# Kernel optimization log

Measured on AMD Instinct MI355X. Metric: run time of the kernel, lower is better.

The kernel has to match this reference:

```python
import jax, jax.numpy as jnp
import numpy as np

N = 50000      # nodes
E = 800000     # edges
G = 2000       # graphs
F_IN = 34
HID = 256
H = 8
D = 32         # HID // H
L = 5


def _layer_norm(x, g, b, eps=1e-5):
    m = x.mean(-1, keepdims=True)
    v = ((x - m) ** 2).mean(-1, keepdims=True)
    return (x - m) / jnp.sqrt(v + eps) * g + b


def _gelu(x):
    return jax.nn.gelu(x, approximate=False)  # torch exact GELU


def _segment_softmax(scores, seg, n):
    # scores: [E', H], seg: [E'] target node ids
    m = jax.ops.segment_max(scores, seg, num_segments=n)
    m = jnp.where(jnp.isfinite(m), m, 0.0)
    ex = jnp.exp(scores - m[seg])
    den = jax.ops.segment_sum(ex, seg, num_segments=n)
    return ex / (den[seg] + 1e-16)


def setup_inputs() -> dict:
    key = jax.random.key(0)
    ks = iter(jax.random.split(key, 64))

    def p(shape, fan):
        return (jax.random.normal(next(ks), shape, jnp.float32) / np.sqrt(fan)).astype(jnp.float32)

    inp = {}
    inp['x'] = jax.random.normal(next(ks), (N, F_IN), jnp.float32)
    inp['edge_index'] = jax.random.randint(next(ks), (2, E), 0, N, jnp.int32)
    inp['batch'] = jnp.sort(jax.random.randint(next(ks), (N,), 0, G, jnp.int32))

    # input embed
    inp['in_W'] = p((F_IN, HID), F_IN); inp['in_b'] = jnp.zeros((HID,), jnp.float32)
    inp['in_ln_g'] = jnp.ones((HID,), jnp.float32); inp['in_ln_b'] = jnp.zeros((HID,), jnp.float32)
    # 5 GATv2 layers (stacked on leading dim)
    inp['gat_Wl'] = p((L, HID, HID), HID); inp['gat_bl'] = jnp.zeros((L, HID), jnp.float32)
    inp['gat_Wr'] = p((L, HID, HID), HID); inp['gat_br'] = jnp.zeros((L, HID), jnp.float32)
    inp['gat_att'] = p((L, H, D), D)
    inp['gat_bias'] = jnp.zeros((L, HID), jnp.float32)
    inp['gat_ln_g'] = jnp.ones((L, HID), jnp.float32); inp['gat_ln_b'] = jnp.zeros((L, HID), jnp.float32)
    # TransformerConv
    inp['tr_Wq'] = p((HID, HID), HID); inp['tr_bq'] = jnp.zeros((HID,), jnp.float32)
    inp['tr_Wk'] = p((HID, HID), HID); inp['tr_bk'] = jnp.zeros((HID,), jnp.float32)
    inp['tr_Wv'] = p((HID, HID), HID); inp['tr_bv'] = jnp.zeros((HID,), jnp.float32)
    inp['tr_Wskip'] = p((HID, HID), HID); inp['tr_bskip'] = jnp.zeros((HID,), jnp.float32)
    inp['tr_ln_g'] = jnp.ones((HID,), jnp.float32); inp['tr_ln_b'] = jnp.zeros((HID,), jnp.float32)
    # output proj
    inp['out_W'] = p((2 * HID, 2 * HID), 2 * HID); inp['out_b'] = jnp.zeros((2 * HID,), jnp.float32)
    inp['out_ln_g'] = jnp.ones((2 * HID,), jnp.float32); inp['out_ln_b'] = jnp.zeros((2 * HID,), jnp.float32)
    return inp


def reference(x, edge_index, batch,
              in_W, in_b, in_ln_g, in_ln_b,
              gat_Wl, gat_bl, gat_Wr, gat_br, gat_att, gat_bias, gat_ln_g, gat_ln_b,
              tr_Wq, tr_bq, tr_Wk, tr_bk, tr_Wv, tr_bv, tr_Wskip, tr_bskip, tr_ln_g, tr_ln_b,
              out_W, out_b, out_ln_g, out_ln_b):
    # input embedding (dropout inactive in eval)
    h = _gelu(_layer_norm(x @ in_W + in_b, in_ln_g, in_ln_b))

    src, dst = edge_index[0], edge_index[1]  # PyG: row=source j, col=target i
    loops = jnp.arange(N, dtype=src.dtype)
    s2 = jnp.concatenate([src, loops])  # GATv2 adds self loops
    d2 = jnp.concatenate([dst, loops])

    for l in range(L):  # small fixed loop over layers
        xl = (h @ gat_Wl[l] + gat_bl[l]).reshape(N, H, D)  # source transform / message
        xr = (h @ gat_Wr[l] + gat_br[l]).reshape(N, H, D)  # target transform
        e = jax.nn.leaky_relu(xl[s2] + xr[d2], 0.2)        # [E', H, D]
        score = jnp.einsum('ehd,hd->eh', e, gat_att[l])
        alpha = _segment_softmax(score, d2, N)             # softmax over incoming edges
        out = jax.ops.segment_sum(xl[s2] * alpha[..., None], d2, num_segments=N)
        out = out.reshape(N, HID) + gat_bias[l]
        h = h + _gelu(_layer_norm(out, gat_ln_g[l], gat_ln_b[l]))

    # TransformerConv (no self loops, root_weight skip connection)
    q = (h @ tr_Wq + tr_bq).reshape(N, H, D)
    k = (h @ tr_Wk + tr_bk).reshape(N, H, D)
    v = (h @ tr_Wv + tr_bv).reshape(N, H, D)
    score = (q[dst] * k[src]).sum(-1) / jnp.sqrt(jnp.float32(D))  # [E, H]
    alpha = _segment_softmax(score, dst, N)
    out = jax.ops.segment_sum(v[src] * alpha[..., None], dst, num_segments=N).reshape(N, HID)
    out = out + h @ tr_Wskip + tr_bskip
    h = h + _layer_norm(out, tr_ln_g, tr_ln_b)

    # global mean + max pool
    cnt = jax.ops.segment_sum(jnp.ones((N,), h.dtype), batch, num_segments=G)
    h_mean = jax.ops.segment_sum(h, batch, num_segments=G) / jnp.maximum(cnt, 1.0)[:, None]
    h_max = jax.ops.segment_max(h, batch, num_segments=G)
    h_max = jnp.where(jnp.isfinite(h_max), h_max, 0.0)
    ge = jnp.concatenate([h_mean, h_max], axis=-1)  # [G, 512]
    return _gelu(_layer_norm(ge @ out_W + out_b, out_ln_g, out_ln_b))
```

## Files before the change

### kernel.cpp

```cpp
#include <hip/hip_runtime.h>
#include <math.h>

#define N_NODES 50000
#define N_EDGES 800000
#define N_GRAPH 2000
#define F_INPUT 34
#define HID 256
#define NLAYER 5

typedef __attribute__((ext_vector_type(8))) short short8;
typedef __attribute__((ext_vector_type(4))) float float4v;

__device__ __forceinline__ float gelu_f(float x) {
  return 0.5f * x * (1.0f + erff(x * 0.70710678118654752440f));
}
__device__ __forceinline__ unsigned short bfr(float f) {
  unsigned u = __float_as_uint(f);
  return (unsigned short)((u + 0x7fffu + ((u >> 16) & 1u)) >> 16);
}
__device__ __forceinline__ float b2f(unsigned short s) {
  return __uint_as_float(((unsigned)s) << 16);
}
__device__ __forceinline__ float b2f_lo(unsigned u) {
  return __uint_as_float(u << 16);
}
__device__ __forceinline__ float b2f_hi(unsigned u) {
  return __uint_as_float(u & 0xffff0000u);
}
__device__ __forceinline__ float4 ld4bf(const unsigned short* p) {
  ushort4 u = *(const ushort4*)p;
  float4 f;
  f.x = b2f(u.x); f.y = b2f(u.y); f.z = b2f(u.z); f.w = b2f(u.w);
  return f;
}
__device__ __forceinline__ void acp16(const unsigned short* g, unsigned short* l) {
  __builtin_amdgcn_global_load_lds(
      (const __attribute__((address_space(1))) void*)g,
      (__attribute__((address_space(3))) void*)l, 16, 0, 0);
}

__global__ __launch_bounds__(256) void gemm_bias(
    const float* __restrict__ A, const float* __restrict__ B,
    const float* __restrict__ bias, float* __restrict__ C,
    int M, int Nn, int K) {
  __shared__ float As[16][64];
  __shared__ float Bs[16][64];
  int tid = threadIdx.x;
  int tx = tid & 15, ty = tid >> 4;
  int row0 = blockIdx.y * 64;
  int col0 = blockIdx.x * 64;
  float acc[4][4] = {};
  int a_r = tid >> 2;
  int a_c = (tid & 3) * 4;
  int b_r = tid >> 4;
  int b_c = (tid & 15) * 4;

  for (int k0 = 0; k0 < K; k0 += 16) {
    int ar = row0 + a_r;
#pragma unroll
    for (int i = 0; i < 4; ++i) {
      int kc = k0 + a_c + i;
      As[a_c + i][a_r] = (ar < M && kc < K) ? A[(long)ar * K + kc] : 0.f;
    }
    int bk = k0 + b_r;
    if (bk < K) {
      float4 bv = *(const float4*)&B[(long)bk * Nn + col0 + b_c];
      Bs[b_r][b_c + 0] = bv.x; Bs[b_r][b_c + 1] = bv.y;
      Bs[b_r][b_c + 2] = bv.z; Bs[b_r][b_c + 3] = bv.w;
    } else {
      Bs[b_r][b_c + 0] = 0.f; Bs[b_r][b_c + 1] = 0.f;
      Bs[b_r][b_c + 2] = 0.f; Bs[b_r][b_c + 3] = 0.f;
    }
    __syncthreads();
#pragma unroll
    for (int kk = 0; kk < 16; ++kk) {
      float4 a = *(const float4*)&As[kk][ty * 4];
      float4 b = *(const float4*)&Bs[kk][tx * 4];
      float av[4] = {a.x, a.y, a.z, a.w};
      float bv[4] = {b.x, b.y, b.z, b.w};
#pragma unroll
      for (int i = 0; i < 4; ++i)
#pragma unroll
        for (int j = 0; j < 4; ++j) acc[i][j] += av[i] * bv[j];
    }
    __syncthreads();
  }
  float4 bi = *(const float4*)&bias[col0 + tx * 4];
  float bia[4] = {bi.x, bi.y, bi.z, bi.w};
#pragma unroll
  for (int i = 0; i < 4; ++i) {
    int r = row0 + ty * 4 + i;
    if (r < M) {
      float4 o;
      o.x = acc[i][0] + bia[0]; o.y = acc[i][1] + bia[1];
      o.z = acc[i][2] + bia[2]; o.w = acc[i][3] + bia[3];
      *(float4*)&C[(long)r * Nn + col0 + tx * 4] = o;
    }
  }
}

__global__ __launch_bounds__(256) void gemm_mfma(
    const unsigned short* __restrict__ A, const unsigned short* __restrict__ Bt,
    const float* __restrict__ bias, void* __restrict__ Cv,
    int M, int Nn, int K, int flags) {
  __shared__ unsigned short smem[12288];
  unsigned short* As = smem;
  unsigned short* Bs = smem + 4096;
  int tid = threadIdx.x;
  int wave = tid >> 6, lane = tid & 63;

  int gx = gridDim.x;
  int flat = blockIdx.y * gx + blockIdx.x;
  int nwg = gx * gridDim.y;
  int xcd = flat & 7, idx = flat >> 3;
  int qb = nwg >> 3, r = nwg & 7;
  int g0 = xcd * qb + min(xcd, r);
  int wk = g0 + idx;
  int row0 = (wk / gx) * 128;
  int col0 = (wk % gx) * 128;

  int wm0 = (wave >> 1) * 64;
  int wn0 = (wave & 1) * 64;
  int q = lane >> 4;
  int ln = lane & 15;

  int srow = wave * 16 + (lane >> 2);
  int scol = (lane & 3) * 8;
  int ra0 = min(row0 + srow, M - 1);
  int ra1 = min(row0 + srow + 64, M - 1);
  const unsigned short* pa0 = A + (size_t)ra0 * K + scol;
  const unsigned short* pa1 = A + (size_t)ra1 * K + scol;
  const unsigned short* pb0 = Bt + (size_t)(col0 + srow) * K + scol;
  const unsigned short* pb1 = Bt + (size_t)(col0 + srow + 64) * K + scol;
  unsigned short* la0 = As + wave * 512;
  unsigned short* la1 = As + wave * 512 + 2048;
  unsigned short* lb0 = Bs + wave * 512;
  unsigned short* lb1 = Bs + wave * 512 + 2048;

  float4v acc[4][4];
#pragma unroll
  for (int i = 0; i < 4; ++i)
#pragma unroll
    for (int j = 0; j < 4; ++j) acc[i][j] = (float4v)0.f;

  for (int k0 = 0; k0 < K; k0 += 32) {
    acp16(pa0 + k0, la0);
    acp16(pa1 + k0, la1);
    acp16(pb0 + k0, lb0);
    acp16(pb1 + k0, lb1);
    __syncthreads();
    short8 af[4], bf[4];
#pragma unroll
    for (int i = 0; i < 4; ++i)
      af[i] = *(const short8*)&As[(wm0 + i * 16 + ln) * 32 + q * 8];
#pragma unroll
    for (int j = 0; j < 4; ++j)
      bf[j] = *(const short8*)&Bs[(wn0 + j * 16 + ln) * 32 + q * 8];
#pragma unroll
    for (int i = 0; i < 4; ++i)
#pragma unroll
      for (int j = 0; j < 4; ++j)
        acc[i][j] = __builtin_amdgcn_mfma_f32_16x16x32_bf16(af[i], bf[j], acc[i][j], 0, 0, 0);
    __syncthreads();
  }
  int rb = (lane >> 4) * 4;
  if (flags & 2) {
    unsigned short* Cb = (unsigned short*)Cv;
    unsigned short* eb = smem + wave * 2560;
#pragma unroll
    for (int p = 0; p < 2; ++p) {
#pragma unroll
      for (int jj = 0; jj < 2; ++jj) {
        int j = p * 2 + jj;
        float bv = bias[col0 + wn0 + j * 16 + ln];
#pragma unroll
        for (int i = 0; i < 4; ++i)
#pragma unroll
          for (int r2 = 0; r2 < 4; ++r2)
            eb[(i * 16 + rb + r2) * 40 + jj * 16 + ln] = bfr(acc[i][j][r2] + bv);
      }
      int grow = row0 + wm0 + lane;
      uint4 w0 = *(uint4*)&eb[lane * 40 + 0];
      uint4 w1 = *(uint4*)&eb[lane * 40 + 8];
      uint4 w2 = *(uint4*)&eb[lane * 40 + 16];
      uint4 w3 = *(uint4*)&eb[lane * 40 + 24];
      if (grow < M) {
        unsigned short* dst = Cb + (size_t)grow * Nn + col0 + wn0 + p * 32;
        *(uint4*)&dst[0] = w0;
        *(uint4*)&dst[8] = w1;
        *(uint4*)&dst[16] = w2;
        *(uint4*)&dst[24] = w3;
      }
    }
  } else {
    float* C = (float*)Cv;
#pragma unroll
    for (int j = 0; j < 4; ++j) {
      int col = col0 + wn0 + j * 16 + ln;
      float bv = bias[col];
#pragma unroll
      for (int i = 0; i < 4; ++i)
#pragma unroll
        for (int r2 = 0; r2 < 4; ++r2) {
          int row = row0 + wm0 + i * 16 + rb + r2;
          if (row < M) C[(size_t)row * Nn + col] = acc[i][j][r2] + bv;
        }
    }
  }
}

__global__ __launch_bounds__(256) void prep_w(
    const float* __restrict__ Wl, const float* __restrict__ Wr,
    const float* __restrict__ Wq, const float* __restrict__ Wk,
    const float* __restrict__ Wv, const float* __restrict__ Wsk,
    unsigned short* __restrict__ out) {
  __shared__ float t[32][33];
  int m = blockIdx.z;
  const float* W = (m < 10) ? (((m & 1) ? Wr : Wl) + (size_t)(m >> 1) * 65536)
                 : (m == 10) ? Wq : (m == 11) ? Wk : (m == 12) ? Wv : Wsk;
  int k0 = blockIdx.y * 32, n0 = blockIdx.x * 32;
  int r = threadIdx.x >> 5, c = threadIdx.x & 31;
  for (int rr = r; rr < 32; rr += 8)
    t[rr][c] = W[(size_t)(k0 + rr) * HID + n0 + c];
  __syncthreads();
  for (int rr = r; rr < 32; rr += 8) {
    int n = n0 + rr;
    size_t row;
    if (m == 11)      row = 11 * 256 + (size_t)((n >> 2) * 8 + (n & 3));
    else if (m == 12) row = 11 * 256 + (size_t)((n >> 2) * 8 + 4 + (n & 3));
    else              row = (size_t)m * 256 + n;
    out[row * HID + k0 + c] = bfr(t[c][rr]);
  }
}

__global__ __launch_bounds__(256) void prep_wout(const float* __restrict__ W,
                                                 unsigned short* __restrict__ o) {
  __shared__ float t[32][33];
  int k0 = blockIdx.y * 32, n0 = blockIdx.x * 32;
  int r = threadIdx.x >> 5, c = threadIdx.x & 31;
  for (int rr = r; rr < 32; rr += 8)
    t[rr][c] = W[(size_t)(k0 + rr) * 512 + n0 + c];
  __syncthreads();
  for (int rr = r; rr < 32; rr += 8)
    o[(size_t)(n0 + rr) * 512 + k0 + c] = bfr(t[c][rr]);
}

__global__ __launch_bounds__(256) void prep_bias(
    const float* __restrict__ bl, const float* __restrict__ br,
    const float* __restrict__ bq, const float* __restrict__ bk,
    const float* __restrict__ bv, const float* __restrict__ bsk,
    float* __restrict__ out) {
  int i = blockIdx.x * 256 + threadIdx.x;
  if (i < 2560) {
    int l = i >> 9, c = i & 511;
    out[i] = (c < 256) ? bl[l * 256 + c] : br[l * 256 + (c - 256)];
  } else if (i < 3584) {
    int j = i - 2560;
    float v;
    if (j < 256) {
      v = bq[j];
    } else if (j < 768) {
      int p = j - 256;
      int hi = p >> 3, lo = p & 7;
      v = (lo < 4) ? bk[hi * 4 + lo] : bv[hi * 4 + (lo - 4)];
    } else {
      v = bsk[j - 768];
    }
    out[i] = v;
  }
}

__global__ __launch_bounds__(256) void ln_act(
    const float* __restrict__ in, const float* __restrict__ gam,
    const float* __restrict__ bet, float* __restrict__ out,
    unsigned short* __restrict__ outb,
    int n_rows, int width, int do_gelu) {
  int wid = blockIdx.x * 4 + (threadIdx.x >> 6);
  int lane = threadIdx.x & 63;
  if (wid >= n_rows) return;
  int chunks = width >> 8;
  float4 v[2];
  float s = 0.f;
  for (int c = 0; c < chunks; ++c) {
    int off = c * 256 + lane * 4;
    float4 t = *(const float4*)&in[(size_t)wid * width + off];
    v[c] = t;
    s += t.x + t.y + t.z + t.w;
  }
  for (int o = 1; o < 64; o <<= 1) s += __shfl_xor(s, o);
  float mean = s / (float)width;
  float vs = 0.f;
  for (int c = 0; c < chunks; ++c) {
    float dx = v[c].x - mean, dy = v[c].y - mean, dz = v[c].z - mean, dw = v[c].w - mean;
    vs += dx * dx + dy * dy + dz * dz + dw * dw;
  }
  for (int o = 1; o < 64; o <<= 1) vs += __shfl_xor(vs, o);
  float inv = rsqrtf(vs / (float)width + 1e-5f);
  for (int c = 0; c < chunks; ++c) {
    int off = c * 256 + lane * 4;
    float4 g4 = *(const float4*)&gam[off];
    float4 b4 = *(const float4*)&bet[off];
    float y[4] = {(v[c].x - mean) * inv * g4.x + b4.x,
                  (v[c].y - mean) * inv * g4.y + b4.y,
                  (v[c].z - mean) * inv * g4.z + b4.z,
                  (v[c].w - mean) * inv * g4.w + b4.w};
    if (do_gelu) {
#pragma unroll
      for (int i = 0; i < 4; ++i) y[i] = gelu_f(y[i]);
    }
    size_t idx = (size_t)wid * width + off;
    float4 o4 = {y[0], y[1], y[2], y[3]};
    *(float4*)&out[idx] = o4;
    if (outb) {
      ushort4 ob = {bfr(y[0]), bfr(y[1]), bfr(y[2]), bfr(y[3])};
      *(ushort4*)&outb[idx] = ob;
    }
  }
}

__global__ __launch_bounds__(256) void edge_count(const int* __restrict__ ei,
                                                  int* __restrict__ counts) {
  int e = blockIdx.x * 256 + threadIdx.x;
  if (e < N_EDGES) atomicAdd(&counts[ei[N_EDGES + e]], 1);
}

__global__ __launch_bounds__(1024) void scan1(const int* __restrict__ counts,
                                              int* __restrict__ indptr,
                                              int* __restrict__ bsums, int n) {
  __shared__ int sm[1024];
  int tid = threadIdx.x;
  int i = blockIdx.x * 1024 + tid;
  int v = (i < n) ? counts[i] : 0;
  sm[tid] = v;
  __syncthreads();
  for (int off = 1; off < 1024; off <<= 1) {
    int t = (tid >= off) ? sm[tid - off] : 0;
    __syncthreads();
    sm[tid] += t;
    __syncthreads();
  }
  if (i < n) indptr[i] = sm[tid] - v;
  if (tid == 1023) bsums[blockIdx.x] = sm[1023];
}

__global__ void scan2(int* __restrict__ bsums, int nb) {
  if (threadIdx.x == 0 && blockIdx.x == 0) {
    int acc = 0;
    for (int i = 0; i < nb; ++i) { int t = bsums[i]; bsums[i] = acc; acc += t; }
  }
}

__global__ __launch_bounds__(256) void scan3(const int* __restrict__ bsums,
                                             int* __restrict__ indptr,
                                             int* __restrict__ cursor, int n) {
  int i = blockIdx.x * 256 + threadIdx.x;
  if (i < n) {
    int v = indptr[i] + bsums[i >> 10];
    indptr[i] = v;
    cursor[i] = v;
  }
  if (i == 0) indptr[n] = N_EDGES;
}

__global__ __launch_bounds__(256) void edge_scatter(const int* __restrict__ ei,
                                                    int* __restrict__ cursor,
                                                    int* __restrict__ esrc) {
  int e = blockIdx.x * 256 + threadIdx.x;
  if (e < N_EDGES) {
    int d = ei[N_EDGES + e];
    int p = atomicAdd(&cursor[d], 1);
    esrc[p] = ei[e];
  }
}

#define GAT_EDGE(f)                                                        \
  {                                                                        \
    float ex = f.x + xri.x; ex = fmaxf(ex, 0.2f * ex);                     \
    float ey = f.y + xri.y; ey = fmaxf(ey, 0.2f * ey);                     \
    float ez = f.z + xri.z; ez = fmaxf(ez, 0.2f * ez);                     \
    float ew = f.w + xri.w; ew = fmaxf(ew, 0.2f * ew);                     \
    float p = ex * a4.x + ey * a4.y + ez * a4.z + ew * a4.w;               \
    p += __shfl_xor(p, 1); p += __shfl_xor(p, 2); p += __shfl_xor(p, 4);   \
    float wgt = __expf(fminf(p - m0, 60.f));                               \
    ax = fmaf(wgt, f.x, ax); ay = fmaf(wgt, f.y, ay);                      \
    az = fmaf(wgt, f.z, az); aw = fmaf(wgt, f.w, aw);                      \
    lsum += wgt;                                                           \
  }

__global__ __launch_bounds__(256) void gat_agg(
    const unsigned short* __restrict__ xlr, const float* __restrict__ att,
    const int* __restrict__ indptr, const int* __restrict__ esrc,
    const float* __restrict__ pre_bias, const float* __restrict__ gam,
    const float* __restrict__ bet, float* __restrict__ h,
    unsigned short* __restrict__ hb) {
  int wid = blockIdx.x * 4 + (threadIdx.x >> 6);
  int lane = threadIdx.x & 63;
  if (wid >= N_NODES) return;
  float4 xri = ld4bf(&xlr[(size_t)wid * 512 + 256 + lane * 4]);
  float4 a4 = *(const float4*)&att[lane * 4];
  int beg = indptr[wid], end = indptr[wid + 1];

  float m0, lsum, ax, ay, az, aw;
  {
    float4 f = ld4bf(&xlr[(size_t)wid * 512 + lane * 4]);
    float ex = f.x + xri.x; ex = fmaxf(ex, 0.2f * ex);
    float ey = f.y + xri.y; ey = fmaxf(ey, 0.2f * ey);
    float ez = f.z + xri.z; ez = fmaxf(ez, 0.2f * ez);
    float ew = f.w + xri.w; ew = fmaxf(ew, 0.2f * ew);
    float p = ex * a4.x + ey * a4.y + ez * a4.z + ew * a4.w;
    p += __shfl_xor(p, 1); p += __shfl_xor(p, 2); p += __shfl_xor(p, 4);
    m0 = p; lsum = 1.f;
    ax = f.x; ay = f.y; az = f.z; aw = f.w;
  }
  const unsigned short* xbase = xlr + lane * 4;
  int e = beg;
  for (; e + 3 < end; e += 4) {
    int j0 = esrc[e], j1 = esrc[e + 1], j2 = esrc[e + 2], j3 = esrc[e + 3];
    float4 f0 = ld4bf(xbase + (size_t)j0 * 512);
    float4 f1 = ld4bf(xbase + (size_t)j1 * 512);
    float4 f2 = ld4bf(xbase + (size_t)j2 * 512);
    float4 f3 = ld4bf(xbase + (size_t)j3 * 512);
    GAT_EDGE(f0); GAT_EDGE(f1); GAT_EDGE(f2); GAT_EDGE(f3);
  }
  for (; e < end; ++e) {
    int j = esrc[e];
    float4 f = ld4bf(xbase + (size_t)j * 512);
    GAT_EDGE(f);
  }
  float inv = 1.f / (lsum + 1e-16f);
  float4 pb = *(const float4*)&pre_bias[lane * 4];
  float y0 = ax * inv + pb.x, y1 = ay * inv + pb.y;
  float y2 = az * inv + pb.z, y3 = aw * inv + pb.w;
  float s = y0 + y1 + y2 + y3;
  for (int o = 1; o < 64; o <<= 1) s += __shfl_xor(s, o);
  float mean = s * (1.f / 256.f);
  float d0 = y0 - mean, d1 = y1 - mean, d2 = y2 - mean, d3 = y3 - mean;
  float vs = d0 * d0 + d1 * d1 + d2 * d2 + d3 * d3;
  for (int o = 1; o < 64; o <<= 1) vs += __shfl_xor(vs, o);
  float inv2 = rsqrtf(vs * (1.f / 256.f) + 1e-5f);
  float4 g4 = *(const float4*)&gam[lane * 4];
  float4 b4 = *(const float4*)&bet[lane * 4];
  y0 = gelu_f(d0 * inv2 * g4.x + b4.x);
  y1 = gelu_f(d1 * inv2 * g4.y + b4.y);
  y2 = gelu_f(d2 * inv2 * g4.z + b4.z);
  y3 = gelu_f(d3 * inv2 * g4.w + b4.w);
  size_t idx = (size_t)wid * HID + lane * 4;
  float4 r4 = *(const float4*)&h[idx];
  y0 += r4.x; y1 += r4.y; y2 += r4.z; y3 += r4.w;
  float4 o4 = {y0, y1, y2, y3};
  *(float4*)&h[idx] = o4;
  ushort4 ob = {bfr(y0), bfr(y1), bfr(y2), bfr(y3)};
  *(ushort4*)&hb[idx] = ob;
}

#define TR_EDGE(u_)                                                         \
  {                                                                         \
    float p = qi.x * b2f_lo(u_.x);                                          \
    p = fmaf(qi.y, b2f_hi(u_.x), p);                                        \
    p = fmaf(qi.z, b2f_lo(u_.y), p);                                        \
    p = fmaf(qi.w, b2f_hi(u_.y), p);                                        \
    p += __shfl_xor(p, 1); p += __shfl_xor(p, 2); p += __shfl_xor(p, 4);    \
    float wgt = __expf(fminf(p, 60.f));                                     \
    ax = fmaf(wgt, b2f_lo(u_.z), ax); ay = fmaf(wgt, b2f_hi(u_.z), ay);     \
    az = fmaf(wgt, b2f_lo(u_.w), az); aw = fmaf(wgt, b2f_hi(u_.w), aw);     \
    lsum += wgt;                                                            \
  }

__global__ __launch_bounds__(256) void tr_agg(
    const unsigned short* __restrict__ qkv, const int* __restrict__ indptr,
    const int* __restrict__ esrc,
    const float* __restrict__ gam, const float* __restrict__ bet,
    float* __restrict__ h) {
  int wid = blockIdx.x * 4 + (threadIdx.x >> 6);
  int lane = threadIdx.x & 63;
  if (wid >= N_NODES) return;
  const float scale = 0.17677669529663687f;
  float4 qi = ld4bf(&qkv[(size_t)wid * 1024 + lane * 4]);
  qi.x *= scale; qi.y *= scale; qi.z *= scale; qi.w *= scale;
  const unsigned short* kvbase = qkv + 256 + lane * 8;
  int beg = indptr[wid], end = indptr[wid + 1];
  float lsum = 0.f;
  float ax = 0.f, ay = 0.f, az = 0.f, aw = 0.f;
  int e = beg;
  for (; e + 3 < end; e += 4) {
    int j0 = esrc[e], j1 = esrc[e + 1], j2 = esrc[e + 2], j3 = esrc[e + 3];
    uint4 u0 = *(const uint4*)(kvbase + (size_t)j0 * 1024);
    uint4 u1 = *(const uint4*)(kvbase + (size_t)j1 * 1024);
    uint4 u2 = *(const uint4*)(kvbase + (size_t)j2 * 1024);
    uint4 u3 = *(const uint4*)(kvbase + (size_t)j3 * 1024);
    TR_EDGE(u0); TR_EDGE(u1); TR_EDGE(u2); TR_EDGE(u3);
  }
  for (; e < end; ++e) {
    uint4 u0 = *(const uint4*)(kvbase + (size_t)esrc[e] * 1024);
    TR_EDGE(u0);
  }
  float inv = 1.f / (lsum + 1e-16f);
  size_t idx = (size_t)wid * HID + lane * 4;
  float4 sk = ld4bf(&qkv[(size_t)wid * 1024 + 768 + lane * 4]);
  float y0 = ax * inv + sk.x, y1 = ay * inv + sk.y;
  float y2 = az * inv + sk.z, y3 = aw * inv + sk.w;
  float s = y0 + y1 + y2 + y3;
  for (int o = 1; o < 64; o <<= 1) s += __shfl_xor(s, o);
  float mean = s * (1.f / 256.f);
  float d0 = y0 - mean, d1 = y1 - mean, d2 = y2 - mean, d3 = y3 - mean;
  float vs = d0 * d0 + d1 * d1 + d2 * d2 + d3 * d3;
  for (int o = 1; o < 64; o <<= 1) vs += __shfl_xor(vs, o);
  float inv2 = rsqrtf(vs * (1.f / 256.f) + 1e-5f);
  float4 g4 = *(const float4*)&gam[lane * 4];
  float4 b4 = *(const float4*)&bet[lane * 4];
  float4 r4 = *(const float4*)&h[idx];
  float4 o4;
  o4.x = r4.x + d0 * inv2 * g4.x + b4.x;
  o4.y = r4.y + d1 * inv2 * g4.y + b4.y;
  o4.z = r4.z + d2 * inv2 * g4.z + b4.z;
  o4.w = r4.w + d3 * inv2 * g4.w + b4.w;
  *(float4*)&h[idx] = o4;
}

__global__ __launch_bounds__(256) void graph_bounds(const int* __restrict__ batch,
                                                    int* __restrict__ gptr) {
  int i = blockIdx.x * 256 + threadIdx.x;
  if (i >= N_NODES) return;
  int b0 = batch[i];
  if (i == 0)
    for (int g = 0; g <= b0; ++g) gptr[g] = 0;
  int b1 = (i + 1 < N_NODES) ? batch[i + 1] : N_GRAPH;
  for (int g = b0 + 1; g <= b1; ++g) gptr[g] = i + 1;
}

__global__ __launch_bounds__(256) void pool_seg(
    const float* __restrict__ h, const int* __restrict__ gptr,
    unsigned short* __restrict__ geb) {
  int g = blockIdx.x, c = threadIdx.x;
  int s = gptr[g], e = gptr[g + 1];
  float sum = 0.f, mx = -INFINITY;
  for (int r = s; r < e; ++r) {
    float vv = h[(size_t)r * HID + c];
    sum += vv;
    mx = fmaxf(mx, vv);
  }
  int cnt = e - s;
  geb[(size_t)g * 512 + c] = bfr(sum / (float)max(cnt, 1));
  geb[(size_t)g * 512 + 256 + c] = bfr(cnt ? mx : 0.f);
}

static inline void mfma_launch(const unsigned short* A, const unsigned short* Bt,
                               const float* bias, void* C, int M, int Nn, int K,
                               int flags, hipStream_t s) {
  dim3 grid(Nn / 128, (M + 127) / 128);
  gemm_mfma<<<grid, 256, 0, s>>>(A, Bt, bias, C, M, Nn, K, flags);
}

extern "C" void kernel_launch(void* const* d_in, const int* in_sizes, int n_in,
                              void* d_out, int out_size, void* d_ws, size_t ws_size,
                              hipStream_t stream) {
  const float* x       = (const float*)d_in[0];
  const int*   ei      = (const int*)d_in[1];
  const int*   batch   = (const int*)d_in[2];
  const float* in_W    = (const float*)d_in[3];
  const float* in_b    = (const float*)d_in[4];
  const float* in_ln_g = (const float*)d_in[5];
  const float* in_ln_b = (const float*)d_in[6];
  const float* gat_Wl  = (const float*)d_in[7];
  const float* gat_bl  = (const float*)d_in[8];
  const float* gat_Wr  = (const float*)d_in[9];
  const float* gat_br  = (const float*)d_in[10];
  const float* gat_att = (const float*)d_in[11];
  const float* gat_bias= (const float*)d_in[12];
  const float* gat_ln_g= (const float*)d_in[13];
  const float* gat_ln_b= (const float*)d_in[14];
  const float* tr_Wq   = (const float*)d_in[15];
  const float* tr_bq   = (const float*)d_in[16];
  const float* tr_Wk   = (const float*)d_in[17];
  const float* tr_bk   = (const float*)d_in[18];
  const float* tr_Wv   = (const float*)d_in[19];
  const float* tr_bv   = (const float*)d_in[20];
  const float* tr_Wsk  = (const float*)d_in[21];
  const float* tr_bsk  = (const float*)d_in[22];
  const float* tr_ln_g = (const float*)d_in[23];
  const float* tr_ln_b = (const float*)d_in[24];
  const float* out_W   = (const float*)d_in[25];
  const float* out_b   = (const float*)d_in[26];
  const float* out_ln_g= (const float*)d_in[27];
  const float* out_ln_b= (const float*)d_in[28];

  char* w = (char*)d_ws;
  auto take = [&](size_t bytes) -> char* {
    char* p = w;
    w += (bytes + 255) & ~(size_t)255;
    return p;
  };
  const size_t NB = (size_t)N_NODES * HID * sizeof(float);
  float* h    = (float*)take(NB);
  float* aggO = (float*)take(NB);
  unsigned short* hb  = (unsigned short*)take((size_t)N_NODES * HID * 2);
  unsigned short* xq  = (unsigned short*)take((size_t)N_NODES * 1024 * 2);
  unsigned short* wbuf= (unsigned short*)take((size_t)(14 * 65536 + 262144) * 2);
  float* bcat = (float*)take(3584 * sizeof(float));
  int* indptr = (int*)take((N_NODES + 1) * sizeof(int));
  int* cursor = (int*)take(N_NODES * sizeof(int));
  int* counts = (int*)take(N_NODES * sizeof(int));
  int* esrc   = (int*)take(N_EDGES * sizeof(int));
  int* bsums  = (int*)take(64 * sizeof(int));
  char* w2 = (char*)xq;
  auto take2 = [&](size_t bytes) -> char* {
    char* p = w2;
    w2 += (bytes + 255) & ~(size_t)255;
    return p;
  };
  int* gptr = (int*)take2((N_GRAPH + 1) * sizeof(int));
  unsigned short* geb = (unsigned short*)take2((size_t)N_GRAPH * 512 * 2);
  float* tbuf = (float*)take2((size_t)N_GRAPH * 512 * sizeof(float));

  const int EB = (N_EDGES + 255) / 256;
  const int WB = (N_NODES + 3) / 4;
  const int NSB = (N_NODES + 1023) / 1024;

  {
    dim3 g(8, 8, 14);
    prep_w<<<g, 256, 0, stream>>>(gat_Wl, gat_Wr, tr_Wq, tr_Wk, tr_Wv, tr_Wsk, wbuf);
    dim3 g2(16, 16);
    prep_wout<<<g2, 256, 0, stream>>>(out_W, wbuf + (size_t)14 * 65536);
    prep_bias<<<14, 256, 0, stream>>>(gat_bl, gat_br, tr_bq, tr_bk, tr_bv, tr_bsk, bcat);
  }

  hipMemsetAsync(counts, 0, N_NODES * sizeof(int), stream);
  edge_count<<<EB, 256, 0, stream>>>(ei, counts);
  scan1<<<NSB, 1024, 0, stream>>>(counts, indptr, bsums, N_NODES);
  scan2<<<1, 64, 0, stream>>>(bsums, NSB);
  scan3<<<(N_NODES + 255) / 256, 256, 0, stream>>>(bsums, indptr, cursor, N_NODES);
  edge_scatter<<<EB, 256, 0, stream>>>(ei, cursor, esrc);

  {
    dim3 grid(HID / 64, (N_NODES + 63) / 64);
    gemm_bias<<<grid, 256, 0, stream>>>(x, in_W, in_b, aggO, N_NODES, HID, F_INPUT);
  }
  ln_act<<<WB, 256, 0, stream>>>(aggO, in_ln_g, in_ln_b, h, hb, N_NODES, HID, 1);

  for (int l = 0; l < NLAYER; ++l) {
    mfma_launch(hb, wbuf + (size_t)(2 * l) * 65536, bcat + l * 512, xq,
                N_NODES, 512, HID, 2, stream);
    gat_agg<<<WB, 256, 0, stream>>>(xq, gat_att + l * HID, indptr, esrc,
                                    gat_bias + l * HID, gat_ln_g + l * HID,
                                    gat_ln_b + l * HID, h, hb);
  }

  mfma_launch(hb, wbuf + (size_t)10 * 65536, bcat + 2560, xq,
              N_NODES, 1024, HID, 2, stream);
  tr_agg<<<WB, 256, 0, stream>>>(xq, indptr, esrc, tr_ln_g, tr_ln_b, h);

  graph_bounds<<<(N_NODES + 255) / 256, 256, 0, stream>>>(batch, gptr);
  pool_seg<<<N_GRAPH, 256, 0, stream>>>(h, gptr, geb);

  mfma_launch(geb, wbuf + (size_t)14 * 65536, out_b, tbuf,
              N_GRAPH, 512, 512, 0, stream);
  ln_act<<<(N_GRAPH + 3) / 4, 256, 0, stream>>>(tbuf, out_ln_g, out_ln_b,
                                                (float*)d_out, nullptr,
                                                N_GRAPH, 512, 1);
}
```

Baseline: 1.138 ms.

## Fuse input embed with layernorm, deepen MFMA K tile, merge prep and scan kernels

Replaces the generic fp32 input GEMM plus separate layernorm/GELU pass with one fused kernel that computes the 34-wide projection, layernorm and GELU per 16-row tile, removing an intermediate N×256 buffer round trip. The MFMA GEMM now stages a 64-wide K slice per iteration, halving barrier count at the cost of more LDS. The three weight and bias prep kernels are merged into one launch, and the single-thread scan2 is folded into scan3, where each block sums its preceding block totals. These cut launch overhead and memory traffic but add redundant prefix work per block.

```diff
diff --git a/kernel.cpp b/kernel.cpp
--- a/kernel.cpp
+++ b/kernel.cpp
@@ -39,63 +39,66 @@
       (__attribute__((address_space(3))) void*)l, 16, 0, 0);
 }
 
-__global__ __launch_bounds__(256) void gemm_bias(
-    const float* __restrict__ A, const float* __restrict__ B,
-    const float* __restrict__ bias, float* __restrict__ C,
-    int M, int Nn, int K) {
-  __shared__ float As[16][64];
-  __shared__ float Bs[16][64];
+__global__ __launch_bounds__(256) void embed_fused(
+    const float* __restrict__ x, const float* __restrict__ W,
+    const float* __restrict__ bias, const float* __restrict__ gam,
+    const float* __restrict__ bet, float* __restrict__ h,
+    unsigned short* __restrict__ hb) {
+  __shared__ float xs[16][34];
+  __shared__ float ys[16][256];
   int tid = threadIdx.x;
-  int tx = tid & 15, ty = tid >> 4;
-  int row0 = blockIdx.y * 64;
-  int col0 = blockIdx.x * 64;
-  float acc[4][4] = {};
-  int a_r = tid >> 2;
-  int a_c = (tid & 3) * 4;
-  int b_r = tid >> 4;
-  int b_c = (tid & 15) * 4;
-
-  for (int k0 = 0; k0 < K; k0 += 16) {
-    int ar = row0 + a_r;
-#pragma unroll
-    for (int i = 0; i < 4; ++i) {
-      int kc = k0 + a_c + i;
-      As[a_c + i][a_r] = (ar < M && kc < K) ? A[(long)ar * K + kc] : 0.f;
-    }
-    int bk = k0 + b_r;
-    if (bk < K) {
-      float4 bv = *(const float4*)&B[(long)bk * Nn + col0 + b_c];
-      Bs[b_r][b_c + 0] = bv.x; Bs[b_r][b_c + 1] = bv.y;
-      Bs[b_r][b_c + 2] = bv.z; Bs[b_r][b_c + 3] = bv.w;
-    } else {
-      Bs[b_r][b_c + 0] = 0.f; Bs[b_r][b_c + 1] = 0.f;
-      Bs[b_r][b_c + 2] = 0.f; Bs[b_r][b_c + 3] = 0.f;
-    }
-    __syncthreads();
-#pragma unroll
-    for (int kk = 0; kk < 16; ++kk) {
-      float4 a = *(const float4*)&As[kk][ty * 4];
-      float4 b = *(const float4*)&Bs[kk][tx * 4];
-      float av[4] = {a.x, a.y, a.z, a.w};
-      float bv[4] = {b.x, b.y, b.z, b.w};
-#pragma unroll
-      for (int i = 0; i < 4; ++i)
-#pragma unroll
-        for (int j = 0; j < 4; ++j) acc[i][j] += av[i] * bv[j];
-    }
-    __syncthreads();
-  }
-  float4 bi = *(const float4*)&bias[col0 + tx * 4];
-  float bia[4] = {bi.x, bi.y, bi.z, bi.w};
-#pragma unroll
-  for (int i = 0; i < 4; ++i) {
-    int r = row0 + ty * 4 + i;
-    if (r < M) {
-      float4 o;
-      o.x = acc[i][0] + bia[0]; o.y = acc[i][1] + bia[1];
-      o.z = acc[i][2] + bia[2]; o.w = acc[i][3] + bia[3];
-      *(float4*)&C[(long)r * Nn + col0 + tx * 4] = o;
-    }
+  int r0 = blockIdx.x * 16;
+  float* xsf = &xs[0][0];
+  for (int i = tid; i < 544; i += 256) xsf[i] = x[(size_t)r0 * 34 + i];
+  __syncthreads();
+  {
+    int rr = tid >> 4;
+    int c0 = (tid & 15) * 16;
+    float acc[16];
+#pragma unroll
+    for (int j = 0; j < 16; j += 4) {
+      float4 b4 = *(const float4*)&bias[c0 + j];
+      acc[j] = b4.x; acc[j + 1] = b4.y; acc[j + 2] = b4.z; acc[j + 3] = b4.w;
+    }
+    for (int k = 0; k < 34; ++k) {
+      float xv = xs[rr][k];
+#pragma unroll
+      for (int j = 0; j < 16; j += 4) {
+        float4 w4 = *(const float4*)&W[(size_t)k * 256 + c0 + j];
+        acc[j]     = fmaf(xv, w4.x, acc[j]);
+        acc[j + 1] = fmaf(xv, w4.y, acc[j + 1]);
+        acc[j + 2] = fmaf(xv, w4.z, acc[j + 2]);
+        acc[j + 3] = fmaf(xv, w4.w, acc[j + 3]);
+      }
+    }
+#pragma unroll
+    for (int j = 0; j < 16; j += 4) {
+      float4 o = {acc[j], acc[j + 1], acc[j + 2], acc[j + 3]};
+      *(float4*)&ys[rr][c0 + j] = o;
+    }
+  }
+  __syncthreads();
+  int wv = tid >> 6, lane = tid & 63;
+  for (int rr = wv * 4; rr < wv * 4 + 4; ++rr) {
+    float4 v = *(const float4*)&ys[rr][lane * 4];
+    float s = v.x + v.y + v.z + v.w;
+    for (int o = 1; o < 64; o <<= 1) s += __shfl_xor(s, o);
+    float mean = s * (1.f / 256.f);
+    float d0 = v.x - mean, d1 = v.y - mean, d2 = v.z - mean, d3 = v.w - mean;
+    float vs = d0 * d0 + d1 * d1 + d2 * d2 + d3 * d3;
+    for (int o = 1; o < 64; o <<= 1) vs += __shfl_xor(vs, o);
+    float inv = rsqrtf(vs * (1.f / 256.f) + 1e-5f);
+    float4 g4 = *(const float4*)&gam[lane * 4];
+    float4 b4 = *(const float4*)&bet[lane * 4];
+    float y0 = gelu_f(d0 * inv * g4.x + b4.x);
+    float y1 = gelu_f(d1 * inv * g4.y + b4.y);
+    float y2 = gelu_f(d2 * inv * g4.z + b4.z);
+    float y3 = gelu_f(d3 * inv * g4.w + b4.w);
+    size_t idx = (size_t)(r0 + rr) * HID + lane * 4;
+    float4 o4 = {y0, y1, y2, y3};
+    *(float4*)&h[idx] = o4;
+    ushort4 ob = {bfr(y0), bfr(y1), bfr(y2), bfr(y3)};
+    *(ushort4*)&hb[idx] = ob;
   }
 }
 
@@ -103,9 +106,9 @@
     const unsigned short* __restrict__ A, const unsigned short* __restrict__ Bt,
     const float* __restrict__ bias, void* __restrict__ Cv,
     int M, int Nn, int K, int flags) {
-  __shared__ unsigned short smem[12288];
+  __shared__ unsigned short smem[16384];
   unsigned short* As = smem;
-  unsigned short* Bs = smem + 4096;
+  unsigned short* Bs = smem + 8192;
   int tid = threadIdx.x;
   int wave = tid >> 6, lane = tid & 63;
 
@@ -124,18 +127,20 @@
   int q = lane >> 4;
   int ln = lane & 15;
 
-  int srow = wave * 16 + (lane >> 2);
-  int scol = (lane & 3) * 8;
-  int ra0 = min(row0 + srow, M - 1);
-  int ra1 = min(row0 + srow + 64, M - 1);
-  const unsigned short* pa0 = A + (size_t)ra0 * K + scol;
-  const unsigned short* pa1 = A + (size_t)ra1 * K + scol;
-  const unsigned short* pb0 = Bt + (size_t)(col0 + srow) * K + scol;
-  const unsigned short* pb1 = Bt + (size_t)(col0 + srow + 64) * K + scol;
-  unsigned short* la0 = As + wave * 512;
-  unsigned short* la1 = As + wave * 512 + 2048;
-  unsigned short* lb0 = Bs + wave * 512;
-  unsigned short* lb1 = Bs + wave * 512 + 2048;
+  int srow = wave * 8 + (lane >> 3);
+  int scol = (lane & 7) * 8;
+  const unsigned short* pa[4];
+  const unsigned short* pb[4];
+  unsigned short* la[4];
+  unsigned short* lb[4];
+#pragma unroll
+  for (int i = 0; i < 4; ++i) {
+    int ra = min(row0 + srow + i * 32, M - 1);
+    pa[i] = A + (size_t)ra * K + scol;
+    pb[i] = Bt + (size_t)(col0 + srow + i * 32) * K + scol;
+    la[i] = As + (i * 32 + wave * 8) * 64;
+    lb[i] = Bs + (i * 32 + wave * 8) * 64;
+  }
 
   float4v acc[4][4];
 #pragma unroll
@@ -143,24 +148,27 @@
 #pragma unroll
     for (int j = 0; j < 4; ++j) acc[i][j] = (float4v)0.f;
 
-  for (int k0 = 0; k0 < K; k0 += 32) {
-    acp16(pa0 + k0, la0);
-    acp16(pa1 + k0, la1);
-    acp16(pb0 + k0, lb0);
-    acp16(pb1 + k0, lb1);
+  for (int k0 = 0; k0 < K; k0 += 64) {
+#pragma unroll
+    for (int i = 0; i < 4; ++i) acp16(pa[i] + k0, la[i]);
+#pragma unroll
+    for (int i = 0; i < 4; ++i) acp16(pb[i] + k0, lb[i]);
     __syncthreads();
-    short8 af[4], bf[4];
-#pragma unroll
-    for (int i = 0; i < 4; ++i)
-      af[i] = *(const short8*)&As[(wm0 + i * 16 + ln) * 32 + q * 8];
-#pragma unroll
-    for (int j = 0; j < 4; ++j)
-      bf[j] = *(const short8*)&Bs[(wn0 + j * 16 + ln) * 32 + q * 8];
-#pragma unroll
-    for (int i = 0; i < 4; ++i)
+#pragma unroll
+    for (int ks = 0; ks < 2; ++ks) {
+      short8 af[4], bf[4];
+#pragma unroll
+      for (int i = 0; i < 4; ++i)
+        af[i] = *(const short8*)&As[(wm0 + i * 16 + ln) * 64 + ks * 32 + q * 8];
 #pragma unroll
       for (int j = 0; j < 4; ++j)
-        acc[i][j] = __builtin_amdgcn_mfma_f32_16x16x32_bf16(af[i], bf[j], acc[i][j], 0, 0, 0);
+        bf[j] = *(const short8*)&Bs[(wn0 + j * 16 + ln) * 64 + ks * 32 + q * 8];
+#pragma unroll
+      for (int i = 0; i < 4; ++i)
+#pragma unroll
+        for (int j = 0; j < 4; ++j)
+          acc[i][j] = __builtin_amdgcn_mfma_f32_16x16x32_bf16(af[i], bf[j], acc[i][j], 0, 0, 0);
+    }
     __syncthreads();
   }
   int rb = (lane >> 4) * 4;
@@ -209,64 +217,62 @@
   }
 }
 
-__global__ __launch_bounds__(256) void prep_w(
+__global__ __launch_bounds__(256) void prep_all(
     const float* __restrict__ Wl, const float* __restrict__ Wr,
     const float* __restrict__ Wq, const float* __restrict__ Wk,
     const float* __restrict__ Wv, const float* __restrict__ Wsk,
-    unsigned short* __restrict__ out) {
-  __shared__ float t[32][33];
-  int m = blockIdx.z;
-  const float* W = (m < 10) ? (((m & 1) ? Wr : Wl) + (size_t)(m >> 1) * 65536)
-                 : (m == 10) ? Wq : (m == 11) ? Wk : (m == 12) ? Wv : Wsk;
-  int k0 = blockIdx.y * 32, n0 = blockIdx.x * 32;
-  int r = threadIdx.x >> 5, c = threadIdx.x & 31;
-  for (int rr = r; rr < 32; rr += 8)
-    t[rr][c] = W[(size_t)(k0 + rr) * HID + n0 + c];
-  __syncthreads();
-  for (int rr = r; rr < 32; rr += 8) {
-    int n = n0 + rr;
-    size_t row;
-    if (m == 11)      row = 11 * 256 + (size_t)((n >> 2) * 8 + (n & 3));
-    else if (m == 12) row = 11 * 256 + (size_t)((n >> 2) * 8 + 4 + (n & 3));
-    else              row = (size_t)m * 256 + n;
-    out[row * HID + k0 + c] = bfr(t[c][rr]);
-  }
-}
-
-__global__ __launch_bounds__(256) void prep_wout(const float* __restrict__ W,
-                                                 unsigned short* __restrict__ o) {
-  __shared__ float t[32][33];
-  int k0 = blockIdx.y * 32, n0 = blockIdx.x * 32;
-  int r = threadIdx.x >> 5, c = threadIdx.x & 31;
-  for (int rr = r; rr < 32; rr += 8)
-    t[rr][c] = W[(size_t)(k0 + rr) * 512 + n0 + c];
-  __syncthreads();
-  for (int rr = r; rr < 32; rr += 8)
-    o[(size_t)(n0 + rr) * 512 + k0 + c] = bfr(t[c][rr]);
-}
-
-__global__ __launch_bounds__(256) void prep_bias(
+    unsigned short* __restrict__ outw,
+    const float* __restrict__ Wout, unsigned short* __restrict__ outwout,
     const float* __restrict__ bl, const float* __restrict__ br,
     const float* __restrict__ bq, const float* __restrict__ bk,
     const float* __restrict__ bv, const float* __restrict__ bsk,
-    float* __restrict__ out) {
-  int i = blockIdx.x * 256 + threadIdx.x;
-  if (i < 2560) {
-    int l = i >> 9, c = i & 511;
-    out[i] = (c < 256) ? bl[l * 256 + c] : br[l * 256 + (c - 256)];
-  } else if (i < 3584) {
-    int j = i - 2560;
-    float v;
-    if (j < 256) {
-      v = bq[j];
-    } else if (j < 768) {
-      int p = j - 256;
-      int hi = p >> 3, lo = p & 7;
-      v = (lo < 4) ? bk[hi * 4 + lo] : bv[hi * 4 + (lo - 4)];
-    } else {
-      v = bsk[j - 768];
-    }
-    out[i] = v;
+    float* __restrict__ bcat) {
+  __shared__ float t[32][33];
+  int z = blockIdx.z;
+  int rr0 = threadIdx.x >> 5, c = threadIdx.x & 31;
+  if (z < 14) {
+    if (blockIdx.x >= 8 || blockIdx.y >= 8) return;
+    const float* W = (z < 10) ? (((z & 1) ? Wr : Wl) + (size_t)(z >> 1) * 65536)
+                   : (z == 10) ? Wq : (z == 11) ? Wk : (z == 12) ? Wv : Wsk;
+    int k0 = blockIdx.y * 32, n0 = blockIdx.x * 32;
+    for (int rr = rr0; rr < 32; rr += 8)
+      t[rr][c] = W[(size_t)(k0 + rr) * HID + n0 + c];
+    __syncthreads();
+    for (int rr = rr0; rr < 32; rr += 8) {
+      int n = n0 + rr;
+      size_t row;
+      if (z == 11)      row = 11 * 256 + (size_t)((n >> 2) * 8 + (n & 3));
+      else if (z == 12) row = 11 * 256 + (size_t)((n >> 2) * 8 + 4 + (n & 3));
+      else              row = (size_t)z * 256 + n;
+      outw[row * HID + k0 + c] = bfr(t[c][rr]);
+    }
+  } else if (z == 14) {
+    int k0 = blockIdx.y * 32, n0 = blockIdx.x * 32;
+    for (int rr = rr0; rr < 32; rr += 8)
+      t[rr][c] = Wout[(size_t)(k0 + rr) * 512 + n0 + c];
+    __syncthreads();
+    for (int rr = rr0; rr < 32; rr += 8)
+      outwout[(size_t)(n0 + rr) * 512 + k0 + c] = bfr(t[c][rr]);
+  } else {
+    if (blockIdx.y != 0 || blockIdx.x >= 14) return;
+    int i = blockIdx.x * 256 + threadIdx.x;
+    if (i < 2560) {
+      int l = i >> 9, cc = i & 511;
+      bcat[i] = (cc < 256) ? bl[l * 256 + cc] : br[l * 256 + (cc - 256)];
+    } else if (i < 3584) {
+      int j = i - 2560;
+      float v;
+      if (j < 256) {
+        v = bq[j];
+      } else if (j < 768) {
+        int p = j - 256;
+        int hi = p >> 3, lo = p & 7;
+        v = (lo < 4) ? bk[hi * 4 + lo] : bv[hi * 4 + (lo - 4)];
+      } else {
+        v = bsk[j - 768];
+      }
+      bcat[i] = v;
+    }
   }
 }
 
@@ -343,19 +349,20 @@
   if (tid == 1023) bsums[blockIdx.x] = sm[1023];
 }
 
-__global__ void scan2(int* __restrict__ bsums, int nb) {
-  if (threadIdx.x == 0 && blockIdx.x == 0) {
-    int acc = 0;
-    for (int i = 0; i < nb; ++i) { int t = bsums[i]; bsums[i] = acc; acc += t; }
-  }
-}
-
 __global__ __launch_bounds__(256) void scan3(const int* __restrict__ bsums,
                                              int* __restrict__ indptr,
                                              int* __restrict__ cursor, int n) {
+  __shared__ int pre;
   int i = blockIdx.x * 256 + threadIdx.x;
+  if (threadIdx.x == 0) {
+    int nb = blockIdx.x >> 2;
+    int a = 0;
+    for (int j = 0; j < nb; ++j) a += bsums[j];
+    pre = a;
+  }
+  __syncthreads();
   if (i < n) {
-    int v = indptr[i] + bsums[i >> 10];
+    int v = indptr[i] + pre;
     indptr[i] = v;
     cursor[i] = v;
   }
@@ -592,7 +599,6 @@
   };
   const size_t NB = (size_t)N_NODES * HID * sizeof(float);
   float* h    = (float*)take(NB);
-  float* aggO = (float*)take(NB);
   unsigned short* hb  = (unsigned short*)take((size_t)N_NODES * HID * 2);
   unsigned short* xq  = (unsigned short*)take((size_t)N_NODES * 1024 * 2);
   unsigned short* wbuf= (unsigned short*)take((size_t)(14 * 65536 + 262144) * 2);
@@ -617,25 +623,21 @@
   const int NSB = (N_NODES + 1023) / 1024;
 
   {
-    dim3 g(8, 8, 14);
-    prep_w<<<g, 256, 0, stream>>>(gat_Wl, gat_Wr, tr_Wq, tr_Wk, tr_Wv, tr_Wsk, wbuf);
-    dim3 g2(16, 16);
-    prep_wout<<<g2, 256, 0, stream>>>(out_W, wbuf + (size_t)14 * 65536);
-    prep_bias<<<14, 256, 0, stream>>>(gat_bl, gat_br, tr_bq, tr_bk, tr_bv, tr_bsk, bcat);
+    dim3 g(16, 16, 16);
+    prep_all<<<g, 256, 0, stream>>>(gat_Wl, gat_Wr, tr_Wq, tr_Wk, tr_Wv, tr_Wsk,
+                                    wbuf, out_W, wbuf + (size_t)14 * 65536,
+                                    gat_bl, gat_br, tr_bq, tr_bk, tr_bv, tr_bsk,
+                                    bcat);
   }
 
   hipMemsetAsync(counts, 0, N_NODES * sizeof(int), stream);
   edge_count<<<EB, 256, 0, stream>>>(ei, counts);
   scan1<<<NSB, 1024, 0, stream>>>(counts, indptr, bsums, N_NODES);
-  scan2<<<1, 64, 0, stream>>>(bsums, NSB);
   scan3<<<(N_NODES + 255) / 256, 256, 0, stream>>>(bsums, indptr, cursor, N_NODES);
   edge_scatter<<<EB, 256, 0, stream>>>(ei, cursor, esrc);
 
-  {
-    dim3 grid(HID / 64, (N_NODES + 63) / 64);
-    gemm_bias<<<grid, 256, 0, stream>>>(x, in_W, in_b, aggO, N_NODES, HID, F_INPUT);
-  }
-  ln_act<<<WB, 256, 0, stream>>>(aggO, in_ln_g, in_ln_b, h, hb, N_NODES, HID, 1);
+  embed_fused<<<N_NODES / 16, 256, 0, stream>>>(x, in_W, in_b, in_ln_g, in_ln_b,
+                                                h, hb);
 
   for (int l = 0; l < NLAYER; ++l) {
     mfma_launch(hb, wbuf + (size_t)(2 * l) * 65536, bcat + l * 512, xq,
```

Result: slower. 1.171 ms (+2.9%).
